# Kernel tuning notes

Hardware: AMD Instinct MI355X
Metric: run time of the kernel (lower is better)

Reference implementation:

```python
import jax, jax.numpy as jnp
import numpy as np

S = 7
B = 2
C = 20
STEP = 1.0 / 7
LAMBDA_COORD = 5.0
LAMBDA_NOOBJ = 0.5
EPS = 1e-10


def setup_inputs() -> dict:
    key = jax.random.key(0)
    k1, k2, k3 = jax.random.split(key, 3)
    N = 16384
    pred = jax.random.normal(k1, (N, S, S, 5 * B + C), dtype=jnp.float32)
    target = jax.random.uniform(k2, (N, S, S, 5 * B + C), dtype=jnp.float32)
    # are binary indicators shared across the B target boxes of a cell
    obj = (jax.random.uniform(k3, (N, S, S)) < 0.3).astype(jnp.float32)
    target = target.at[..., 4].set(obj)
    target = target.at[..., 9].set(obj)
    return {"pred": pred, "target": target}


def _convert_boxes(box):
    # box: [N, S, S, B, 4] with (x_off, y_off, w, h); grid col index -> x, row index -> y
    gx = jnp.arange(S, dtype=box.dtype).reshape(1, 1, S, 1)  # dim 2 = x (col)
    gy = jnp.arange(S, dtype=box.dtype).reshape(1, S, 1, 1)  # dim 1 = y (row)
    x0 = (box[..., 0] + gx) * STEP - box[..., 2] / 2
    y0 = (box[..., 1] + gy) * STEP - box[..., 3] / 2
    out = jnp.stack([x0, y0, box[..., 2], box[..., 3]], axis=-1)
    return jnp.clip(out, 0.0)  # torch.clamp(box, 0) clamps all entries


def _pairwise_iou(b1, b2):
    # b1, b2: [N, S, S, B, 4] converted corner-format (x0, y0, w, h); IoU per matched box index
    x1, y1, w1, h1 = b1[..., 0], b1[..., 1], b1[..., 2], b1[..., 3]
    x2, y2, w2, h2 = b2[..., 0], b2[..., 1], b2[..., 2], b2[..., 3]
    inter_w = jnp.clip(w1 + w2 - (jnp.maximum(x1 + w1, x2 + w2) - jnp.minimum(x1, x2)), 0.0)
    inter_h = jnp.clip(h1 + h2 - (jnp.maximum(y1 + h1, y2 + h2) - jnp.minimum(y1, y2)), 0.0)
    inter = inter_w * inter_h
    union = w1 * h1 + w2 * h2 - inter
    return inter / (union + EPS)


def reference(pred, target):
    N = pred.shape[0]
    target_boxes = target[..., : 5 * B].reshape(N, S, S, B, 5)
    pred_boxes = pred[..., : 5 * B].reshape(N, S, S, B, 5)
    target_class = target[..., 5 * B :]
    pred_class = pred[..., 5 * B :]

    # cell has an object if target conf of box index 1 is > 0 (sig_mask in original)
    cell_mask = (target_boxes[..., 1, 4] > 0).astype(pred.dtype)  # [N,S,S]

    ious = _pairwise_iou(
        _convert_boxes(pred_boxes[..., :4]),
        _convert_boxes(target_boxes[..., :4]),
    )  # [N,S,S,B]
    ious = jax.lax.stop_gradient(ious)  # .item() in original detaches the IoU target

    max_i = jnp.argmax(ious, axis=-1)  # responsible box per cell
    resp = jax.nn.one_hot(max_i, B, dtype=pred.dtype)  # [N,S,S,B]

    obj_box = cell_mask[..., None] * resp          # responsible boxes in object cells
    noobj_box = 1.0 - obj_box                      # other box + all boxes in empty cells

    coord_loss = LAMBDA_COORD * jnp.sum(
        obj_box[..., None] * (pred_boxes[..., :4] - target_boxes[..., :4]) ** 2
    )
    conf_loss = jnp.sum(obj_box * (pred_boxes[..., 4] - ious) ** 2)
    noobj_loss = LAMBDA_NOOBJ * jnp.sum(noobj_box * pred_boxes[..., 4] ** 2)
    class_loss = jnp.sum(cell_mask[..., None] * (pred_class - target_class) ** 2)

    return (coord_loss + conf_loss + noobj_loss + class_loss) / N
```

## Files before the change

### kernel.cpp

```cpp
#include <hip/hip_runtime.h>


typedef float vfloat4 __attribute__((ext_vector_type(4)));

constexpr int S = 7;
constexpr int FPC = 30;
constexpr int BLK = 256;
constexpr int WAVES = BLK / 64;
constexpr int TILE_F4 = 64 * FPC / 4;
constexpr float STEP = 1.0f / 7.0f;
constexpr float EPS = 1e-10f;

__global__ __launch_bounds__(BLK) void yolo_partial_kernel(
    const float* __restrict__ pred,
    const float* __restrict__ target,
    float* __restrict__ partial) {
  __shared__ float lds[WAVES][64 * FPC];
  __shared__ float wsum[WAVES];

  const int tid = threadIdx.x;
  const int lane = tid & 63;
  const int wid = tid >> 6;
  const int cellw = blockIdx.x * BLK + wid * 64;
  const int cell = cellw + lane;

  float* myld = lds[wid];

  vfloat4 pr[8];
  {
    const vfloat4* g = (const vfloat4*)(pred + (size_t)cellw * FPC);
    #pragma unroll
    for (int it = 0; it < 8; ++it) {
      const int idx = it * 64 + lane;
      if (idx < TILE_F4) pr[it] = g[idx];
    }
  }
  float2 tv[FPC / 2];
  {
    const float2* t2 = (const float2*)(target + (size_t)cell * FPC);
    #pragma unroll
    for (int i = 0; i < FPC / 2; ++i) tv[i] = t2[i];
  }

  {
    vfloat4* l = (vfloat4*)myld;
    #pragma unroll
    for (int it = 0; it < 8; ++it) {
      const int idx = it * 64 + lane;
      if (idx < TILE_F4) l[idx] = pr[it];
    }
  }

  union Buf { float2 v[FPC / 2]; float f[FPC]; };
  Buf P, T;
  {
    const float2* l2 = (const float2*)(myld + lane * FPC);
    #pragma unroll
    for (int i = 0; i < FPC / 2; ++i) P.v[i] = l2[i];
  }
  #pragma unroll
  for (int i = 0; i < FPC / 2; ++i) T.v[i] = tv[i];

  const float* p = P.f;
  const float* t = T.f;

  const float gx = (float)(cell % S);
  const float gy = (float)((cell / S) % S);
  const float mask = (t[9] > 0.0f) ? 1.0f : 0.0f;

  float iou[2];
  #pragma unroll
  for (int b = 0; b < 2; ++b) {
    const float* pb = p + 5 * b;
    const float* tb = t + 5 * b;
    float px = fmaxf((pb[0] + gx) * STEP - pb[2] * 0.5f, 0.0f);
    float py = fmaxf((pb[1] + gy) * STEP - pb[3] * 0.5f, 0.0f);
    float pw = fmaxf(pb[2], 0.0f);
    float ph = fmaxf(pb[3], 0.0f);
    float tx = fmaxf((tb[0] + gx) * STEP - tb[2] * 0.5f, 0.0f);
    float ty = fmaxf((tb[1] + gy) * STEP - tb[3] * 0.5f, 0.0f);
    float tw = fmaxf(tb[2], 0.0f);
    float th = fmaxf(tb[3], 0.0f);
    float iw = fmaxf(pw + tw - (fmaxf(px + pw, tx + tw) - fminf(px, tx)), 0.0f);
    float ih = fmaxf(ph + th - (fmaxf(py + ph, ty + th) - fminf(py, ty)), 0.0f);
    float inter = iw * ih;
    float uni = pw * ph + tw * th - inter;
    iou[b] = inter / (uni + EPS);
  }
  const int best = (iou[1] > iou[0]) ? 1 : 0;

  float loss = 0.0f;
  #pragma unroll
  for (int b = 0; b < 2; ++b) {
    const float* pb = p + 5 * b;
    const float* tb = t + 5 * b;
    float obj = (b == best) ? mask : 0.0f;
    float d0 = pb[0] - tb[0];
    float d1 = pb[1] - tb[1];
    float d2 = pb[2] - tb[2];
    float d3 = pb[3] - tb[3];
    loss += 5.0f * obj * (d0 * d0 + d1 * d1 + d2 * d2 + d3 * d3);
    float dc = pb[4] - iou[b];
    loss += obj * dc * dc;
    loss += 0.5f * (1.0f - obj) * pb[4] * pb[4];
  }
  float cls = 0.0f;
  #pragma unroll
  for (int k = 10; k < 30; ++k) {
    float d = p[k] - t[k];
    cls += d * d;
  }
  loss += mask * cls;

  #pragma unroll
  for (int off = 32; off > 0; off >>= 1)
    loss += __shfl_down(loss, off, 64);
  if ((tid & 63) == 0) wsum[wid] = loss;
  __syncthreads();
  if (tid == 0) {
    float total = 0.0f;
    #pragma unroll
    for (int w = 0; w < WAVES; ++w) total += wsum[w];
    partial[blockIdx.x] = total;
  }
}

__global__ __launch_bounds__(256) void yolo_reduce_kernel(
    const float* __restrict__ partial, float* __restrict__ out,
    int n, float invN) {
  __shared__ float wsum[4];
  const int tid = threadIdx.x;
  float s = 0.0f;
  for (int i = tid; i < n; i += 256) s += partial[i];
  #pragma unroll
  for (int off = 32; off > 0; off >>= 1)
    s += __shfl_down(s, off, 64);
  if ((tid & 63) == 0) wsum[tid >> 6] = s;
  __syncthreads();
  if (tid == 0)
    out[0] = (wsum[0] + wsum[1] + wsum[2] + wsum[3]) * invN;
}

extern "C" void kernel_launch(void* const* d_in, const int* in_sizes, int n_in,
                              void* d_out, int out_size, void* d_ws, size_t ws_size,
                              hipStream_t stream) {
  const float* pred = (const float*)d_in[0];
  const float* target = (const float*)d_in[1];
  float* out = (float*)d_out;
  float* partial = (float*)d_ws;

  const int ncells = in_sizes[0] / FPC;
  const int nblocks = ncells / BLK;
  const float invN = 1.0f / (float)(ncells / (S * S));

  yolo_partial_kernel<<<nblocks, BLK, 0, stream>>>(pred, target, partial);
  yolo_reduce_kernel<<<1, 256, 0, stream>>>(partial, out, nblocks, invN);
}
```

Before: 206.0 us.

## Fuse final reduction via atomic ticket and stage target through LDS with nontemporal loads

The separate reduction kernel is merged into the main kernel: each block takes an atomic ticket after writing its partial sum, and the last block to finish sums all partials and writes the output. The target tensor is now read with coalesced float4 nontemporal loads and transposed through LDS, like pred already was, instead of strided per-thread float2 loads. Pred loads also become nontemporal. A memset launch is added to reset the counter, and the workspace offset for the counter is hardcoded.

Measured after the change: 341.6 us. +65.8%, slower.

```diff
diff --git a/kernel.cpp b/kernel.cpp
--- a/kernel.cpp
+++ b/kernel.cpp
@@ -11,12 +11,16 @@
 constexpr float STEP = 1.0f / 7.0f;
 constexpr float EPS = 1e-10f;
 
-__global__ __launch_bounds__(BLK) void yolo_partial_kernel(
+__global__ __launch_bounds__(BLK) void yolo_fused_kernel(
     const float* __restrict__ pred,
     const float* __restrict__ target,
-    float* __restrict__ partial) {
+    float* __restrict__ partial,
+    unsigned int* __restrict__ ticket_ctr,
+    float* __restrict__ out,
+    int nblocks, float invN) {
   __shared__ float lds[WAVES][64 * FPC];
   __shared__ float wsum[WAVES];
+  __shared__ unsigned int ticket;
 
   const int tid = threadIdx.x;
   const int lane = tid & 63;
@@ -26,21 +30,24 @@
 
   float* myld = lds[wid];
 
-  vfloat4 pr[8];
+  vfloat4 pr[8], tr[8];
   {
-    const vfloat4* g = (const vfloat4*)(pred + (size_t)cellw * FPC);
+    const vfloat4* gp = (const vfloat4*)(pred + (size_t)cellw * FPC);
+    const vfloat4* gt = (const vfloat4*)(target + (size_t)cellw * FPC);
     #pragma unroll
     for (int it = 0; it < 8; ++it) {
       const int idx = it * 64 + lane;
-      if (idx < TILE_F4) pr[it] = g[idx];
+      if (idx < TILE_F4) pr[it] = __builtin_nontemporal_load(gp + idx);
+    }
+    #pragma unroll
+    for (int it = 0; it < 8; ++it) {
+      const int idx = it * 64 + lane;
+      if (idx < TILE_F4) tr[it] = __builtin_nontemporal_load(gt + idx);
     }
   }
-  float2 tv[FPC / 2];
-  {
-    const float2* t2 = (const float2*)(target + (size_t)cell * FPC);
-    #pragma unroll
-    for (int i = 0; i < FPC / 2; ++i) tv[i] = t2[i];
-  }
+
+  union Buf { float2 v[FPC / 2]; float f[FPC]; };
+  Buf P, T;
 
   {
     vfloat4* l = (vfloat4*)myld;
@@ -49,17 +56,22 @@
       const int idx = it * 64 + lane;
       if (idx < TILE_F4) l[idx] = pr[it];
     }
-  }
-
-  union Buf { float2 v[FPC / 2]; float f[FPC]; };
-  Buf P, T;
-  {
     const float2* l2 = (const float2*)(myld + lane * FPC);
     #pragma unroll
     for (int i = 0; i < FPC / 2; ++i) P.v[i] = l2[i];
   }
-  #pragma unroll
-  for (int i = 0; i < FPC / 2; ++i) T.v[i] = tv[i];
+  asm volatile("" ::: "memory");
+  {
+    vfloat4* l = (vfloat4*)myld;
+    #pragma unroll
+    for (int it = 0; it < 8; ++it) {
+      const int idx = it * 64 + lane;
+      if (idx < TILE_F4) l[idx] = tr[it];
+    }
+    const float2* l2 = (const float2*)(myld + lane * FPC);
+    #pragma unroll
+    for (int i = 0; i < FPC / 2; ++i) T.v[i] = l2[i];
+  }
 
   const float* p = P.f;
   const float* t = T.f;
@@ -122,23 +134,25 @@
     #pragma unroll
     for (int w = 0; w < WAVES; ++w) total += wsum[w];
     partial[blockIdx.x] = total;
+    __threadfence();
+    ticket = atomicAdd(ticket_ctr, 1u);
   }
-}
+  __syncthreads();
 
-__global__ __launch_bounds__(256) void yolo_reduce_kernel(
-    const float* __restrict__ partial, float* __restrict__ out,
-    int n, float invN) {
-  __shared__ float wsum[4];
-  const int tid = threadIdx.x;
-  float s = 0.0f;
-  for (int i = tid; i < n; i += 256) s += partial[i];
-  #pragma unroll
-  for (int off = 32; off > 0; off >>= 1)
-    s += __shfl_down(s, off, 64);
-  if ((tid & 63) == 0) wsum[tid >> 6] = s;
-  __syncthreads();
-  if (tid == 0)
-    out[0] = (wsum[0] + wsum[1] + wsum[2] + wsum[3]) * invN;
+  if (ticket == (unsigned)(nblocks - 1)) {
+    __threadfence();
+    float s = 0.0f;
+    for (int i = tid; i < nblocks; i += BLK)
+      s += __hip_atomic_load(&partial[i], __ATOMIC_RELAXED,
+                             __HIP_MEMORY_SCOPE_AGENT);
+    #pragma unroll
+    for (int off = 32; off > 0; off >>= 1)
+      s += __shfl_down(s, off, 64);
+    if ((tid & 63) == 0) wsum[tid >> 6] = s;
+    __syncthreads();
+    if (tid == 0)
+      out[0] = (wsum[0] + wsum[1] + wsum[2] + wsum[3]) * invN;
+  }
 }
 
 extern "C" void kernel_launch(void* const* d_in, const int* in_sizes, int n_in,
@@ -148,11 +162,14 @@
   const float* target = (const float*)d_in[1];
   float* out = (float*)d_out;
   float* partial = (float*)d_ws;
+  unsigned int* ticket_ctr = (unsigned int*)((char*)d_ws + 12544);
 
   const int ncells = in_sizes[0] / FPC;
   const int nblocks = ncells / BLK;
   const float invN = 1.0f / (float)(ncells / (S * S));
 
-  yolo_partial_kernel<<<nblocks, BLK, 0, stream>>>(pred, target, partial);
-  yolo_reduce_kernel<<<1, 256, 0, stream>>>(partial, out, nblocks, invN);
+  hipMemsetAsync(ticket_ctr, 0, sizeof(unsigned int), stream);
+  yolo_fused_kernel<<<nblocks, BLK, 0, stream>>>(pred, target, partial,
+                                                 ticket_ctr, out,
+                                                 nblocks, invN);
 }
```
